# Kernel optimization log

Hardware: AMD Instinct MI355X
Metric: run time of the kernel (lower is better)

The kernel has to match this reference:

```python
import jax, jax.numpy as jnp
import numpy as np

N, C_IN, C_OUT, P, W, H = 32, 32, 16, 4, 16, 16
D = P * P
EPS = 1e-6


def squash(s, axis=-1):
    # v = ||s||^2/(1+||s||^2) * s/||s||, eps-stabilized as in the repo (eps=1e-6)
    n2 = jnp.sum(s * s, axis=axis, keepdims=True)
    n = jnp.sqrt(n2)
    return (n2 / (1.0 + n2)) * s / (n + EPS)


def setup_inputs() -> dict:
    key = jax.random.key(0)
    k1, k2, k3 = jax.random.split(key, 3)
    l = jax.random.normal(k1, (N, C_IN, D, W, H), jnp.float32)
    g = jax.random.normal(k2, (N, C_OUT, D), jnp.float32)
    weight = jax.random.normal(k3, (1, C_IN, 1, C_OUT, P, P), jnp.float32)
    return {"l": l, "g": g, "weight": weight, "num_iters": 3}


def reference(l, g, weight, num_iters):
    n, c, d, w, h = l.shape
    p = weight.shape[-1]
    c_out = weight.shape[3]
    # (N, C, D, W, H) -> (N, C, W*H, P, P)
    lp = jnp.transpose(l, (0, 1, 3, 4, 2)).reshape(n, c, w * h, p, p)
    # votes: pose matmul against per-(in,out) transform matrices
    # v[n,c,s,o] = lp[n,c,s] @ weight[0,c,0,o]   -> (N, C, WH, C_out, P, P)
    v = jnp.einsum('ncsij,cojk->ncsoik', lp, weight[0, :, 0])
    M = c * w * h
    v = v.reshape(n, M, c_out, d)          # (N, M, C_out, D)
    g = g[:, None, :, :]                    # (N, 1, C_out, D)
    # dynamic routing, logits initialized from agreement with the prior global capsule g
    b = jnp.sum(v * g, axis=-1, keepdims=True)   # (N, M, C_out, 1)
    cc = None
    for _ in range(num_iters):
        cc = jax.nn.softmax(b, axis=1)           # attention over input votes M
        g = squash(jnp.sum(cc * v, axis=1, keepdims=True))  # (N, 1, C_out, D)
        b = b + jnp.sum(v * g, axis=-1, keepdims=True)
    a = jnp.squeeze(cc, -1)   # (N, M, C_out)
    g = jnp.squeeze(g, 1)     # (N, C_out, D)
    return a, g
```

## Files before the change

kernel.cpp:

```cpp
#include <hip/hip_runtime.h>
#include <math.h>

#define N_   32
#define CIN  32
#define COUT 16
#define D_   16
#define S_   256
#define M_   (CIN * S_)

#define PART_STRIDE 18
#define LOG2E 1.4426950408889634f

#define WS_G1 0
#define WS_G2 (N_ * COUT * D_)
#define WS_P0 (2 * N_ * COUT * D_)
#define WS_P1 (WS_P0 + N_ * CIN * COUT * PART_STRIDE)

#define SW(s) ((((s) & 3)) ^ (((s) >> 2) & 3))

__device__ __forceinline__ void stage_tile(const float* __restrict__ gsrc,
                                           float* ls, int tid) {
  const float4* src = (const float4*)gsrc;
#pragma unroll
  for (int j = 0; j < 4; j++) {
    int f = ((tid & 3) << 6) + (tid >> 2) + (j << 8);
    float4 val = src[f];
    int dd = f >> 6;
    int u  = f & 63;
    int chunk = dd >> 2, lo = dd & 3;
    float vv[4] = {val.x, val.y, val.z, val.w};
#pragma unroll
    for (int m = 0; m < 4; m++) {
      int s = (u << 2) + m;
      int p = chunk ^ SW(s);
      ls[(s << 4) + (p << 2) + lo] = vv[m];
    }
  }
}

__device__ __forceinline__ void read_lp(const float* ls, int s, float* lp) {
  const float4* row = (const float4*)(ls + (s << 4));
  int sw = SW(s);
#pragma unroll
  for (int c = 0; c < 4; c++) {
    float4 q = row[c ^ sw];
    lp[c * 4 + 0] = q.x; lp[c * 4 + 1] = q.y;
    lp[c * 4 + 2] = q.z; lp[c * 4 + 3] = q.w;
  }
}

__device__ __forceinline__ void merge_in(float& mx, float& se, float* E,
                                         float m2, float s2, const float* E2) {
  float nm = fmaxf(mx, m2);
  float f1 = exp2f(mx - nm);
  float f2 = exp2f(m2 - nm);
  se = se * f1 + s2 * f2;
#pragma unroll
  for (int d = 0; d < 16; d++) E[d] = E[d] * f1 + E2[d] * f2;
  mx = nm;
}

__device__ __forceinline__ void head_reduce(const float* __restrict__ part_n,
                                            int tid,
                                            float (*red)[COUT][PART_STRIDE],
                                            float& mx, float& se, float* S) {
  const int o = tid & 15, cc = tid >> 4;
  const float* p0 = part_n + ((size_t)cc * COUT + o) * PART_STRIDE;
  const float* p1 = part_n + ((size_t)(cc + 16) * COUT + o) * PART_STRIDE;
  mx = p0[0]; se = p0[1];
#pragma unroll
  for (int d = 0; d < 16; d++) S[d] = p0[2 + d];
  {
    float m2 = p1[0], s2 = p1[1], S2[16];
#pragma unroll
    for (int d = 0; d < 16; d++) S2[d] = p1[2 + d];
    merge_in(mx, se, S, m2, s2, S2);
  }
#pragma unroll
  for (int off = 16; off <= 32; off <<= 1) {
    float m2 = __shfl_xor(mx, off);
    float s2 = __shfl_xor(se, off);
    float S2[16];
#pragma unroll
    for (int d = 0; d < 16; d++) S2[d] = __shfl_xor(S[d], off);
    merge_in(mx, se, S, m2, s2, S2);
  }
  const int w = tid >> 6;
  if ((tid & 63) < 16) {
    red[w][o][0] = mx; red[w][o][1] = se;
#pragma unroll
    for (int d = 0; d < 16; d++) red[w][o][2 + d] = S[d];
  }
  __syncthreads();
  mx = red[0][o][0]; se = red[0][o][1];
#pragma unroll
  for (int d = 0; d < 16; d++) S[d] = red[0][o][2 + d];
#pragma unroll
  for (int ww = 1; ww < 4; ww++) {
    float m2 = red[ww][o][0], s2 = red[ww][o][1], S2[16];
#pragma unroll
    for (int d = 0; d < 16; d++) S2[d] = red[ww][o][2 + d];
    merge_in(mx, se, S, m2, s2, S2);
  }
  __syncthreads();
}

__global__ __launch_bounds__(256, 2) void pass_kernel(
    const float* __restrict__ l, const float* __restrict__ wgt,
    const float* __restrict__ g0, const float* __restrict__ gprev,
    float* __restrict__ gstore, const float* __restrict__ part_in,
    float* __restrict__ part_out, int has_head) {
  const int bid = blockIdx.x;
  const int n = bid >> 5;
  const int c = bid & 31;
  const int tid = threadIdx.x;
  const int o = tid & 15;
  const int lane = tid >> 4;

  __shared__ float ls[D_ * S_];
  __shared__ float red[4][COUT][PART_STRIDE];

  stage_tile(l + ((size_t)(n * CIN + c)) * D_ * S_, ls, tid);

  float wreg[16];
  {
    const float4* wp = (const float4*)(wgt + (c * COUT + o) * 16);
#pragma unroll
    for (int i = 0; i < 4; i++) {
      float4 t = wp[i];
      wreg[i * 4 + 0] = t.x; wreg[i * 4 + 1] = t.y;
      wreg[i * 4 + 2] = t.z; wreg[i * 4 + 3] = t.w;
    }
  }

  float Greg[16];
  if (!has_head) {
    const float4* gp = (const float4*)(g0 + (n * COUT + o) * 16);
#pragma unroll
    for (int i = 0; i < 4; i++) {
      float4 u = gp[i];
      Greg[i * 4 + 0] = u.x; Greg[i * 4 + 1] = u.y;
      Greg[i * 4 + 2] = u.z; Greg[i * 4 + 3] = u.w;
    }
  } else {
    float mx, se, S[16];
    head_reduce(part_in + (size_t)n * CIN * COUT * PART_STRIDE, tid, red, mx, se, S);
    float inv = 1.0f / se;
    float Sg[16], n2 = 0.f;
#pragma unroll
    for (int d = 0; d < 16; d++) { Sg[d] = S[d] * inv; n2 = fmaf(Sg[d], Sg[d], n2); }
    float coef = n2 / ((1.f + n2) * (sqrtf(n2) + 1e-6f));
    const float* gp = gprev + (n * COUT + o) * 16;
#pragma unroll
    for (int d = 0; d < 16; d++) Greg[d] = gp[d] + coef * Sg[d];
    if (c == 0 && tid < 16) {
      float* gs = gstore + (n * COUT + tid) * 16;
#pragma unroll
      for (int d = 0; d < 16; d++) gs[d] = Greg[d];
    }
  }

  float WG[16];
#pragma unroll
  for (int i = 0; i < 4; i++)
#pragma unroll
    for (int j = 0; j < 4; j++) {
      float acc = 0.f;
#pragma unroll
      for (int k = 0; k < 4; k++) acc = fmaf(wreg[j * 4 + k], Greg[i * 4 + k], acc);
      WG[i * 4 + j] = acc * LOG2E;
    }

  __syncthreads();

  float mx = -INFINITY, se = 0.f, E[16];
#pragma unroll
  for (int d = 0; d < 16; d++) E[d] = 0.f;

#pragma unroll
  for (int it = 0; it < 16; it++) {
    int s = lane + (it << 4);
    float lp[16];
    read_lp(ls, s, lp);
    float b = 0.f;
#pragma unroll
    for (int d = 0; d < 16; d++) b = fmaf(lp[d], WG[d], b);
    float nm = fmaxf(mx, b);
    float f1 = exp2f(mx - nm);
    float e  = exp2f(b - nm);
    se = se * f1 + e;
#pragma unroll
    for (int d = 0; d < 16; d++) E[d] = fmaf(E[d], f1, e * lp[d]);
    mx = nm;
  }

#pragma unroll
  for (int off = 16; off <= 32; off <<= 1) {
    float m2 = __shfl_xor(mx, off);
    float s2 = __shfl_xor(se, off);
    float E2[16];
#pragma unroll
    for (int d = 0; d < 16; d++) E2[d] = __shfl_xor(E[d], off);
    merge_in(mx, se, E, m2, s2, E2);
  }

  const int w = tid >> 6;
  if ((tid & 63) < 16) {
    red[w][o][0] = mx;
    red[w][o][1] = se;
#pragma unroll
    for (int d = 0; d < 16; d++) red[w][o][2 + d] = E[d];
  }
  __syncthreads();

  if (tid < COUT) {
    float mxt = red[0][tid][0], set = red[0][tid][1], Et[16];
#pragma unroll
    for (int d = 0; d < 16; d++) Et[d] = red[0][tid][2 + d];
#pragma unroll
    for (int ww = 1; ww < 4; ww++) {
      float E2[16];
#pragma unroll
      for (int d = 0; d < 16; d++) E2[d] = red[ww][tid][2 + d];
      merge_in(mxt, set, Et, red[ww][tid][0], red[ww][tid][1], E2);
    }
    float* p = part_out + ((size_t)((n * CIN + c) * COUT + tid)) * PART_STRIDE;
    p[0] = mxt;
    p[1] = set;
#pragma unroll
    for (int i = 0; i < 4; i++)
#pragma unroll
      for (int k = 0; k < 4; k++) {
        float acc = 0.f;
#pragma unroll
        for (int j = 0; j < 4; j++) acc = fmaf(Et[i * 4 + j], wreg[j * 4 + k], acc);
        p[2 + i * 4 + k] = acc;
      }
  }
}

__global__ __launch_bounds__(256, 2) void a_kernel(
    const float* __restrict__ l, const float* __restrict__ wgt,
    const float* __restrict__ g2, const float* __restrict__ part_in,
    float* __restrict__ a_out, float* __restrict__ g_out) {
  const int bid = blockIdx.x;
  const int n = bid >> 5;
  const int c = bid & 31;
  const int tid = threadIdx.x;
  const int o = tid & 15;
  const int lane = tid >> 4;

  __shared__ float ls[D_ * S_];
  __shared__ float red[4][COUT][PART_STRIDE];

  stage_tile(l + ((size_t)(n * CIN + c)) * D_ * S_, ls, tid);

  float wreg[16];
  {
    const float4* wp = (const float4*)(wgt + (c * COUT + o) * 16);
#pragma unroll
    for (int i = 0; i < 4; i++) {
      float4 t = wp[i];
      wreg[i * 4 + 0] = t.x; wreg[i * 4 + 1] = t.y;
      wreg[i * 4 + 2] = t.z; wreg[i * 4 + 3] = t.w;
    }
  }

  float mx, se, S[16];
  head_reduce(part_in + (size_t)n * CIN * COUT * PART_STRIDE, tid, red, mx, se, S);
  const float inv_se = 1.0f / se;

  if (c == 0 && tid < 16) {
    float Sg[16], n2 = 0.f;
#pragma unroll
    for (int d = 0; d < 16; d++) { Sg[d] = S[d] * inv_se; n2 = fmaf(Sg[d], Sg[d], n2); }
    float coef = n2 / ((1.f + n2) * (sqrtf(n2) + 1e-6f));
    float* go = g_out + (n * COUT + tid) * 16;
#pragma unroll
    for (int d = 0; d < 16; d++) go[d] = coef * Sg[d];
  }

  float WG[16];
  {
    float Greg[16];
    const float4* gp = (const float4*)(g2 + (n * COUT + o) * 16);
#pragma unroll
    for (int i = 0; i < 4; i++) {
      float4 u = gp[i];
      Greg[i * 4 + 0] = u.x; Greg[i * 4 + 1] = u.y;
      Greg[i * 4 + 2] = u.z; Greg[i * 4 + 3] = u.w;
    }
#pragma unroll
    for (int i = 0; i < 4; i++)
#pragma unroll
      for (int j = 0; j < 4; j++) {
        float acc = 0.f;
#pragma unroll
        for (int k = 0; k < 4; k++) acc = fmaf(wreg[j * 4 + k], Greg[i * 4 + k], acc);
        WG[i * 4 + j] = acc * LOG2E;
      }
  }

  __syncthreads();

#pragma unroll
  for (int it = 0; it < 16; it++) {
    int s = lane + (it << 4);
    float lp[16];
    read_lp(ls, s, lp);
    float b = 0.f;
#pragma unroll
    for (int d = 0; d < 16; d++) b = fmaf(lp[d], WG[d], b);
    a_out[((size_t)(n * M_ + c * S_ + s)) * COUT + o] = exp2f(b - mx) * inv_se;
  }
}

extern "C" void kernel_launch(void* const* d_in, const int* in_sizes, int n_in,
                              void* d_out, int out_size, void* d_ws, size_t ws_size,
                              hipStream_t stream) {
  const float* l = (const float*)d_in[0];
  const float* g = (const float*)d_in[1];
  const float* w = (const float*)d_in[2];

  float* out = (float*)d_out;
  float* ws = (float*)d_ws;
  float* a_out = out;
  float* g_out = out + (size_t)N_ * M_ * COUT;

  float* G1 = ws + WS_G1;
  float* G2 = ws + WS_G2;
  float* PB0 = ws + WS_P0;
  float* PB1 = ws + WS_P1;

  pass_kernel<<<N_ * CIN, 256, 0, stream>>>(l, w, g, nullptr, nullptr, nullptr, PB0, 0);
  pass_kernel<<<N_ * CIN, 256, 0, stream>>>(l, w, g, g, G1, PB0, PB1, 1);
  pass_kernel<<<N_ * CIN, 256, 0, stream>>>(l, w, g, G1, G2, PB1, PB0, 1);
  a_kernel<<<N_ * CIN, 256, 0, stream>>>(l, w, G2, PB0, a_out, g_out);
}
```

Measured before the change: 132.7 us.

## Dump final routing logits in last pass and normalize them in a light a_kernel

The third routing pass now writes its per-vote logits b straight into the output buffer. The final a_kernel no longer restages l or recomputes logits. It only reduces the partial max and sum-exp stats, then rescales the stored logits in place with coalesced float4 accesses over a wider grid. The pass loop is also split into a logit pass and a two-pass softmax accumulation, with a true max replacing the online rescale. The partials layout becomes component-major for coalesced reads, and launch bounds are raised to 4 blocks. The cost is an extra write and read of the a-sized tensor and higher register pressure from holding 16 logits per thread.

Result: no change. 131.7 us (-0.8%).

```diff
diff --git a/kernel.cpp b/kernel.cpp
--- a/kernel.cpp
+++ b/kernel.cpp
@@ -15,6 +15,8 @@
 #define WS_G2 (N_ * COUT * D_)
 #define WS_P0 (2 * N_ * COUT * D_)
 #define WS_P1 (WS_P0 + N_ * CIN * COUT * PART_STRIDE)
+
+#define PIDX(n, c) (((size_t)((n) * CIN + (c))) * PART_STRIDE * COUT)
 
 #define SW(s) ((((s) & 3)) ^ (((s) >> 2) & 3))
 
@@ -49,6 +51,18 @@
   }
 }
 
+__device__ __forceinline__ float dot16(const float* a, const float* b) {
+  float a0 = 0.f, a1 = 0.f, a2 = 0.f, a3 = 0.f;
+#pragma unroll
+  for (int k = 0; k < 4; k++) {
+    a0 = fmaf(a[k],      b[k],      a0);
+    a1 = fmaf(a[4 + k],  b[4 + k],  a1);
+    a2 = fmaf(a[8 + k],  b[8 + k],  a2);
+    a3 = fmaf(a[12 + k], b[12 + k], a3);
+  }
+  return (a0 + a1) + (a2 + a3);
+}
+
 __device__ __forceinline__ void merge_in(float& mx, float& se, float* E,
                                          float m2, float s2, const float* E2) {
   float nm = fmaxf(mx, m2);
@@ -65,15 +79,15 @@
                                             float (*red)[COUT][PART_STRIDE],
                                             float& mx, float& se, float* S) {
   const int o = tid & 15, cc = tid >> 4;
-  const float* p0 = part_n + ((size_t)cc * COUT + o) * PART_STRIDE;
-  const float* p1 = part_n + ((size_t)(cc + 16) * COUT + o) * PART_STRIDE;
-  mx = p0[0]; se = p0[1];
-#pragma unroll
-  for (int d = 0; d < 16; d++) S[d] = p0[2 + d];
+  const float* pa = part_n + (size_t)cc * PART_STRIDE * COUT + o;
+  const float* pb = part_n + (size_t)(cc + 16) * PART_STRIDE * COUT + o;
+  mx = pa[0]; se = pa[COUT];
+#pragma unroll
+  for (int d = 0; d < 16; d++) S[d] = pa[(2 + d) * COUT];
   {
-    float m2 = p1[0], s2 = p1[1], S2[16];
-#pragma unroll
-    for (int d = 0; d < 16; d++) S2[d] = p1[2 + d];
+    float m2 = pb[0], s2 = pb[COUT], S2[16];
+#pragma unroll
+    for (int d = 0; d < 16; d++) S2[d] = pb[(2 + d) * COUT];
     merge_in(mx, se, S, m2, s2, S2);
   }
 #pragma unroll
@@ -105,11 +119,11 @@
   __syncthreads();
 }
 
-__global__ __launch_bounds__(256, 2) void pass_kernel(
+__global__ __launch_bounds__(256, 4) void pass_kernel(
     const float* __restrict__ l, const float* __restrict__ wgt,
     const float* __restrict__ g0, const float* __restrict__ gprev,
     float* __restrict__ gstore, const float* __restrict__ part_in,
-    float* __restrict__ part_out, int has_head) {
+    float* __restrict__ part_out, float* __restrict__ bdump, int has_head) {
   const int bid = blockIdx.x;
   const int n = bid >> 5;
   const int c = bid & 31;
@@ -144,7 +158,7 @@
     }
   } else {
     float mx, se, S[16];
-    head_reduce(part_in + (size_t)n * CIN * COUT * PART_STRIDE, tid, red, mx, se, S);
+    head_reduce(part_in + PIDX(n, 0), tid, red, mx, se, S);
     float inv = 1.0f / se;
     float Sg[16], n2 = 0.f;
 #pragma unroll
@@ -173,26 +187,38 @@
 
   __syncthreads();
 
-  float mx = -INFINITY, se = 0.f, E[16];
+  float b[16];
+#pragma unroll
+  for (int it = 0; it < 16; it++) {
+    float lp[16];
+    read_lp(ls, lane + (it << 4), lp);
+    b[it] = dot16(lp, WG);
+  }
+  if (bdump) {
+    float* bp = bdump + ((size_t)(n * M_ + c * S_ + lane)) * COUT + o;
+#pragma unroll
+    for (int it = 0; it < 16; it++) bp[(size_t)(it << 4) * COUT] = b[it];
+  }
+  float m8[8];
+#pragma unroll
+  for (int i = 0; i < 8; i++) m8[i] = fmaxf(b[i], b[i + 8]);
+#pragma unroll
+  for (int i = 0; i < 4; i++) m8[i] = fmaxf(m8[i], m8[i + 4]);
+  float mx = fmaxf(fmaxf(m8[0], m8[1]), fmaxf(m8[2], m8[3]));
+
+  float se0 = 0.f, se1 = 0.f, E[16];
 #pragma unroll
   for (int d = 0; d < 16; d++) E[d] = 0.f;
-
 #pragma unroll
   for (int it = 0; it < 16; it++) {
-    int s = lane + (it << 4);
     float lp[16];
-    read_lp(ls, s, lp);
-    float b = 0.f;
-#pragma unroll
-    for (int d = 0; d < 16; d++) b = fmaf(lp[d], WG[d], b);
-    float nm = fmaxf(mx, b);
-    float f1 = exp2f(mx - nm);
-    float e  = exp2f(b - nm);
-    se = se * f1 + e;
-#pragma unroll
-    for (int d = 0; d < 16; d++) E[d] = fmaf(E[d], f1, e * lp[d]);
-    mx = nm;
-  }
+    read_lp(ls, lane + (it << 4), lp);
+    float e = exp2f(b[it] - mx);
+    if (it & 1) se1 += e; else se0 += e;
+#pragma unroll
+    for (int d = 0; d < 16; d++) E[d] = fmaf(e, lp[d], E[d]);
+  }
+  float se = se0 + se1;
 
 #pragma unroll
   for (int off = 16; off <= 32; off <<= 1) {
@@ -224,9 +250,9 @@
       for (int d = 0; d < 16; d++) E2[d] = red[ww][tid][2 + d];
       merge_in(mxt, set, Et, red[ww][tid][0], red[ww][tid][1], E2);
     }
-    float* p = part_out + ((size_t)((n * CIN + c) * COUT + tid)) * PART_STRIDE;
+    float* p = part_out + PIDX(n, c) + tid;
     p[0] = mxt;
-    p[1] = set;
+    p[COUT] = set;
 #pragma unroll
     for (int i = 0; i < 4; i++)
 #pragma unroll
@@ -234,84 +260,85 @@
         float acc = 0.f;
 #pragma unroll
         for (int j = 0; j < 4; j++) acc = fmaf(Et[i * 4 + j], wreg[j * 4 + k], acc);
-        p[2 + i * 4 + k] = acc;
+        p[(2 + i * 4 + k) * COUT] = acc;
       }
   }
 }
 
-__global__ __launch_bounds__(256, 2) void a_kernel(
-    const float* __restrict__ l, const float* __restrict__ wgt,
-    const float* __restrict__ g2, const float* __restrict__ part_in,
-    float* __restrict__ a_out, float* __restrict__ g_out) {
+__global__ __launch_bounds__(256, 4) void a_kernel(
+    const float* __restrict__ part_in, float* __restrict__ a_out,
+    float* __restrict__ g_out) {
   const int bid = blockIdx.x;
-  const int n = bid >> 5;
-  const int c = bid & 31;
+  const int n = bid >> 6;
+  const int chunk = bid & 63;
   const int tid = threadIdx.x;
-  const int o = tid & 15;
-  const int lane = tid >> 4;
-
-  __shared__ float ls[D_ * S_];
+
   __shared__ float red[4][COUT][PART_STRIDE];
-
-  stage_tile(l + ((size_t)(n * CIN + c)) * D_ * S_, ls, tid);
-
-  float wreg[16];
-  {
-    const float4* wp = (const float4*)(wgt + (c * COUT + o) * 16);
-#pragma unroll
-    for (int i = 0; i < 4; i++) {
-      float4 t = wp[i];
-      wreg[i * 4 + 0] = t.x; wreg[i * 4 + 1] = t.y;
-      wreg[i * 4 + 2] = t.z; wreg[i * 4 + 3] = t.w;
-    }
-  }
-
-  float mx, se, S[16];
-  head_reduce(part_in + (size_t)n * CIN * COUT * PART_STRIDE, tid, red, mx, se, S);
-  const float inv_se = 1.0f / se;
-
-  if (c == 0 && tid < 16) {
-    float Sg[16], n2 = 0.f;
-#pragma unroll
-    for (int d = 0; d < 16; d++) { Sg[d] = S[d] * inv_se; n2 = fmaf(Sg[d], Sg[d], n2); }
-    float coef = n2 / ((1.f + n2) * (sqrtf(n2) + 1e-6f));
-    float* go = g_out + (n * COUT + tid) * 16;
-#pragma unroll
-    for (int d = 0; d < 16; d++) go[d] = coef * Sg[d];
-  }
-
-  float WG[16];
-  {
-    float Greg[16];
-    const float4* gp = (const float4*)(g2 + (n * COUT + o) * 16);
-#pragma unroll
-    for (int i = 0; i < 4; i++) {
-      float4 u = gp[i];
-      Greg[i * 4 + 0] = u.x; Greg[i * 4 + 1] = u.y;
-      Greg[i * 4 + 2] = u.z; Greg[i * 4 + 3] = u.w;
-    }
-#pragma unroll
-    for (int i = 0; i < 4; i++)
-#pragma unroll
-      for (int j = 0; j < 4; j++) {
-        float acc = 0.f;
-#pragma unroll
-        for (int k = 0; k < 4; k++) acc = fmaf(wreg[j * 4 + k], Greg[i * 4 + k], acc);
-        WG[i * 4 + j] = acc * LOG2E;
-      }
-  }
-
-  __syncthreads();
-
-#pragma unroll
-  for (int it = 0; it < 16; it++) {
-    int s = lane + (it << 4);
-    float lp[16];
-    read_lp(ls, s, lp);
-    float b = 0.f;
-#pragma unroll
-    for (int d = 0; d < 16; d++) b = fmaf(lp[d], WG[d], b);
-    a_out[((size_t)(n * M_ + c * S_ + s)) * COUT + o] = exp2f(b - mx) * inv_se;
+  __shared__ float r2[4][COUT][2];
+  __shared__ float smx[16], sinv[16];
+
+  const float* pn = part_in + PIDX(n, 0);
+  float mx, se;
+
+  if (chunk == 0) {
+    float S[16];
+    head_reduce(pn, tid, red, mx, se, S);
+    if (tid < 16) {
+      float inv = 1.0f / se;
+      float Sg[16], n2 = 0.f;
+#pragma unroll
+      for (int d = 0; d < 16; d++) { Sg[d] = S[d] * inv; n2 = fmaf(Sg[d], Sg[d], n2); }
+      float coef = n2 / ((1.f + n2) * (sqrtf(n2) + 1e-6f));
+      float* go = g_out + (n * COUT + tid) * 16;
+#pragma unroll
+      for (int d = 0; d < 16; d++) go[d] = coef * Sg[d];
+    }
+  } else {
+    const int o = tid & 15, cc = tid >> 4;
+    const float* pa = pn + (size_t)cc * PART_STRIDE * COUT + o;
+    const float* pb = pn + (size_t)(cc + 16) * PART_STRIDE * COUT + o;
+    mx = pa[0]; se = pa[COUT];
+    {
+      float m2 = pb[0], s2 = pb[COUT];
+      float nm = fmaxf(mx, m2);
+      se = se * exp2f(mx - nm) + s2 * exp2f(m2 - nm);
+      mx = nm;
+    }
+#pragma unroll
+    for (int off = 16; off <= 32; off <<= 1) {
+      float m2 = __shfl_xor(mx, off);
+      float s2 = __shfl_xor(se, off);
+      float nm = fmaxf(mx, m2);
+      se = se * exp2f(mx - nm) + s2 * exp2f(m2 - nm);
+      mx = nm;
+    }
+    const int w = tid >> 6;
+    if ((tid & 63) < 16) { r2[w][o][0] = mx; r2[w][o][1] = se; }
+    __syncthreads();
+    mx = r2[0][o][0]; se = r2[0][o][1];
+#pragma unroll
+    for (int ww = 1; ww < 4; ww++) {
+      float m2 = r2[ww][o][0], s2 = r2[ww][o][1];
+      float nm = fmaxf(mx, m2);
+      se = se * exp2f(mx - nm) + s2 * exp2f(m2 - nm);
+      mx = nm;
+    }
+  }
+
+  if (tid < 16) { smx[tid] = mx; sinv[tid] = 1.0f / se; }
+  __syncthreads();
+
+  float4* pv = (float4*)(a_out + (size_t)n * (M_ * COUT) + (size_t)chunk * 2048);
+#pragma unroll
+  for (int r = 0; r < 2; r++) {
+    int i4 = tid + (r << 8);
+    int o0 = (i4 & 3) << 2;
+    float4 v = pv[i4];
+    v.x = exp2f(v.x - smx[o0 + 0]) * sinv[o0 + 0];
+    v.y = exp2f(v.y - smx[o0 + 1]) * sinv[o0 + 1];
+    v.z = exp2f(v.z - smx[o0 + 2]) * sinv[o0 + 2];
+    v.w = exp2f(v.w - smx[o0 + 3]) * sinv[o0 + 3];
+    pv[i4] = v;
   }
 }
 
@@ -332,8 +359,9 @@
   float* PB0 = ws + WS_P0;
   float* PB1 = ws + WS_P1;
 
-  pass_kernel<<<N_ * CIN, 256, 0, stream>>>(l, w, g, nullptr, nullptr, nullptr, PB0, 0);
-  pass_kernel<<<N_ * CIN, 256, 0, stream>>>(l, w, g, g, G1, PB0, PB1, 1);
-  pass_kernel<<<N_ * CIN, 256, 0, stream>>>(l, w, g, G1, G2, PB1, PB0, 1);
-  a_kernel<<<N_ * CIN, 256, 0, stream>>>(l, w, G2, PB0, a_out, g_out);
-}
+  pass_kernel<<<N_ * CIN, 256, 0, stream>>>(l, w, g, nullptr, nullptr, nullptr,
+                                            PB0, nullptr, 0);
+  pass_kernel<<<N_ * CIN, 256, 0, stream>>>(l, w, g, g, G1, PB0, PB1, nullptr, 1);
+  pass_kernel<<<N_ * CIN, 256, 0, stream>>>(l, w, g, G1, G2, PB1, PB0, a_out, 1);
+  a_kernel<<<N_ * 64, 256, 0, stream>>>(PB0, a_out, g_out);
+}
```
